# Performance work log

Hardware: AMD Instinct MI355X
Metric: run time of the kernel (lower is better)

## Reference

```python
import jax, jax.numpy as jnp
import numpy as np
import math

N_COARSE, N_FINE = 8192, 32768
DEC_DIM, ENC_DIM, OUT_DIM, K = 256, 128, 128, 16
LN_EPS = 1e-5


def setup_inputs() -> dict:
    key = jax.random.key(0)
    ks = jax.random.split(key, 16)
    s = lambda fan_in: 1.0 / math.sqrt(fan_in)
    return {
        "decoder_features": jax.random.normal(ks[0], (N_COARSE, DEC_DIM), jnp.float32),
        "decoder_pos": jax.random.normal(ks[1], (N_COARSE, 3), jnp.float32),
        "encoder_features": jax.random.normal(ks[2], (N_FINE, ENC_DIM), jnp.float32),
        "encoder_pos": jax.random.normal(ks[3], (N_FINE, 3), jnp.float32),
        "encoder_labels": jax.random.randint(ks[4], (N_FINE,), 0, 13, jnp.int64),
        # params (torch nn.Linear default init scale)
        "Wq": jax.random.uniform(ks[5], (DEC_DIM, ENC_DIM), jnp.float32, -s(ENC_DIM), s(ENC_DIM)),
        "bq": jnp.zeros((DEC_DIM,), jnp.float32),
        "Wk": jax.random.uniform(ks[6], (DEC_DIM, DEC_DIM), jnp.float32, -s(DEC_DIM), s(DEC_DIM)),
        "bk": jnp.zeros((DEC_DIM,), jnp.float32),
        "Wv": jax.random.uniform(ks[7], (DEC_DIM, DEC_DIM), jnp.float32, -s(DEC_DIM), s(DEC_DIM)),
        "bv": jnp.zeros((DEC_DIM,), jnp.float32),
        "W1": jax.random.uniform(ks[8], (OUT_DIM, DEC_DIM + ENC_DIM), jnp.float32, -s(DEC_DIM + ENC_DIM), s(DEC_DIM + ENC_DIM)),
        "b1": jnp.zeros((OUT_DIM,), jnp.float32),
        "W2": jax.random.uniform(ks[9], (OUT_DIM, OUT_DIM), jnp.float32, -s(OUT_DIM), s(OUT_DIM)),
        "b2": jnp.zeros((OUT_DIM,), jnp.float32),
        "ln_g": jnp.ones((OUT_DIM,), jnp.float32),
        "ln_b": jnp.zeros((OUT_DIM,), jnp.float32),
    }


def _knn_indices(encoder_pos, decoder_pos, k):
    # For each fine (encoder) point, k nearest coarse (decoder) points.
    # squared distances [N_fine, N_coarse]
    d2 = (
        jnp.sum(encoder_pos * encoder_pos, axis=1, keepdims=True)
        - 2.0 * encoder_pos @ decoder_pos.T
        + jnp.sum(decoder_pos * decoder_pos, axis=1)[None, :]
    )
    _, idx = jax.lax.top_k(-d2, k)  # [N_fine, K]
    return idx


def reference(decoder_features, decoder_pos, encoder_features, encoder_pos,
              encoder_labels, Wq, bq, Wk, bk, Wv, bv, W1, b1, W2, b2, ln_g, ln_b):
    idx = _knn_indices(encoder_pos, decoder_pos, K)            # [Nf, K]
    nbr = decoder_features[idx]                                 # [Nf, K, Dd]
    query = encoder_features @ Wq.T + bq                        # [Nf, Dd]
    keys = nbr @ Wk.T + bk                                      # [Nf, K, Dd]
    values = nbr @ Wv.T + bv                                    # [Nf, K, Dd]
    scores = jnp.einsum('nd,nkd->nk', query, keys) / math.sqrt(DEC_DIM)
    # segment softmax over edges grouped by fine target == softmax over K
    weights = jax.nn.softmax(scores, axis=-1)                   # [Nf, K]
    agg = jnp.einsum('nk,nkd->nd', weights, values)             # [Nf, Dd]
    combined = jnp.concatenate([agg, encoder_features], axis=-1)
    h = jax.nn.relu(combined @ W1.T + b1)
    up = h @ W2.T + b2                                          # [Nf, out]
    mu = jnp.mean(up, axis=-1, keepdims=True)
    var = jnp.var(up, axis=-1, keepdims=True)
    out = (up - mu) * jax.lax.rsqrt(var + LN_EPS) * ln_g + ln_b
    # dropout is identity in eval mode
    return (out, encoder_pos, encoder_labels)
```

## Files before the change

kernel.cpp:

```cpp
#include <hip/hip_runtime.h>
#include <hip/hip_bf16.h>

typedef __hip_bfloat16 bf16;
typedef unsigned short u16;
typedef float f32x2 __attribute__((ext_vector_type(2)));

#define NC 8192
#define NF 32768
#define KNN 16
#define FMAXV 3.402823466e+38f

__device__ __forceinline__ float bfbits2f(u16 u){
  union { unsigned u; float f; } x; x.u = ((unsigned)u) << 16; return x.f;
}
__device__ __forceinline__ float asfloat(unsigned u){
  union { unsigned u; float f; } x; x.u = u; return x.f;
}
__device__ __forceinline__ f32x2 pk_fma(f32x2 a, f32x2 b, f32x2 c){
  f32x2 d;
  asm("v_pk_fma_f32 %0, %1, %2, %3" : "=v"(d) : "v"(a), "v"(b), "v"(c));
  return d;
}

__global__ __launch_bounds__(256) void k_prep(const float* __restrict__ dpos,
                                              const float* __restrict__ W1,
                                              const float* __restrict__ W2,
                                              float4* __restrict__ posP,
                                              float4* __restrict__ W1eSa,
                                              float4* __restrict__ W1eSb,
                                              float4* __restrict__ W2Sa,
                                              float4* __restrict__ W2Sb){
  int g = blockIdx.x * 256 + threadIdx.x;
  if (g < 4096){
    const float2* dp2 = (const float2*)(dpos + (size_t)g * 6);
    float2 a = dp2[0], b = dp2[1], c = dp2[2];
    float x0 = a.x, y0 = a.y, z0 = b.x;
    float x1 = b.y, y1 = c.x, z1 = c.y;
    float dd0 = __fadd_rn(__fadd_rn(__fmul_rn(x0,x0), __fmul_rn(y0,y0)), __fmul_rn(z0,z0));
    float dd1 = __fadd_rn(__fadd_rn(__fmul_rn(x1,x1), __fmul_rn(y1,y1)), __fmul_rn(z1,z1));
    posP[g * 2]     = make_float4(x0, x1, y0, y1);
    posP[g * 2 + 1] = make_float4(z0, z1, dd0 * 0.5f, dd1 * 0.5f);
  } else if (g >= 8192 && g < 10240){
    int f = g - 8192; int c4 = f >> 6, jg = f & 63;
    W1eSa[f] = ((const float4*)(W1 + (size_t)(2 * jg) * 384 + 256))[c4];
  } else if (g >= 10240 && g < 12288){
    int f = g - 10240; int c4 = f >> 6, jg = f & 63;
    W1eSb[f] = ((const float4*)(W1 + (size_t)(2 * jg + 1) * 384 + 256))[c4];
  } else if (g >= 12288 && g < 14336){
    int f = g - 12288; int c4 = f >> 6, jg = f & 63;
    W2Sa[f] = ((const float4*)(W2 + (size_t)(2 * jg) * 128))[c4];
  } else if (g >= 14336){
    int f = g - 14336; int c4 = f >> 6, jg = f & 63;
    W2Sb[f] = ((const float4*)(W2 + (size_t)(2 * jg + 1) * 128))[c4];
  }
}

__global__ __launch_bounds__(256) void k_wprod(const float* __restrict__ Wk,
                                               const float* __restrict__ Wv,
                                               const float* __restrict__ Wq,
                                               const float* __restrict__ W1,
                                               const float* __restrict__ bk,
                                               const float* __restrict__ bv,
                                               const float* __restrict__ bq,
                                               float* __restrict__ WkqS,
                                               float* __restrict__ WvuS,
                                               float* __restrict__ bkq,
                                               float* __restrict__ bvu,
                                               float* __restrict__ wbq,
                                               float* __restrict__ sbq){
  __shared__ float partial[256];
  __shared__ float red[256];
  int B = blockIdx.x, t = threadIdx.x;
  int csel = B >> 2, tch = B & 3;
  int o = (t & 63) + tch * 64;
  int q = t >> 6;
  int j0 = q * 64;
  if (csel < 128){
    int c = csel;
    float acc = 0.f;
    for (int j = j0; j < j0 + 64; ++j)
      acc = fmaf(Wk[(size_t)j * 256 + o], Wq[(size_t)j * 128 + c], acc);
    partial[t] = acc;
    if (tch == 0) red[t] = bk[t] * Wq[(size_t)t * 128 + c];
    __syncthreads();
    if (t < 64){
      float a = partial[t] + partial[t + 64] + partial[t + 128] + partial[t + 192];
      WkqS[(size_t)((o >> 2) * 128 + c) * 4 + (o & 3)] = a;
    }
    if (tch == 0){
      for (int s = 128; s > 0; s >>= 1){ if (t < s) red[t] += red[t + s]; __syncthreads(); }
      if (t == 0) bkq[c] = red[0];
    }
  } else if (csel < 256){
    int h = csel - 128;
    float acc = 0.f;
    for (int j = j0; j < j0 + 64; ++j)
      acc = fmaf(Wv[(size_t)j * 256 + o], W1[(size_t)h * 384 + j], acc);
    partial[t] = acc;
    if (tch == 0) red[t] = bv[t] * W1[(size_t)h * 384 + t];
    __syncthreads();
    if (t < 64){
      float a = partial[t] + partial[t + 64] + partial[t + 128] + partial[t + 192];
      WvuS[(size_t)((o >> 2) * 128 + h) * 4 + (o & 3)] = a;
    }
    if (tch == 0){
      for (int s = 128; s > 0; s >>= 1){ if (t < s) red[t] += red[t + s]; __syncthreads(); }
      if (t == 0) bvu[h] = red[0];
    }
  } else {
    float acc = 0.f;
    for (int j = j0; j < j0 + 64; ++j)
      acc = fmaf(Wk[(size_t)j * 256 + o], bq[j], acc);
    partial[t] = acc;
    if (tch == 0) red[t] = bk[t] * bq[t];
    __syncthreads();
    if (t < 64){
      float a = partial[t] + partial[t + 64] + partial[t + 128] + partial[t + 192];
      wbq[o] = a;
    }
    if (tch == 0){
      for (int s = 128; s > 0; s >>= 1){ if (t < s) red[t] += red[t + s]; __syncthreads(); }
      if (t == 0) sbq[0] = red[0];
    }
  }
}

__global__ __launch_bounds__(256) void k_dec(const float* __restrict__ df,
                                             const float4* __restrict__ WkqS,
                                             const float4* __restrict__ WvuS,
                                             const float* __restrict__ bkq,
                                             const float* __restrict__ bvu,
                                             const float* __restrict__ wbq,
                                             const float* __restrict__ sbq,
                                             bf16* __restrict__ Zd, bf16* __restrict__ Ud,
                                             float* __restrict__ bqK){
  __shared__ float part[8][32];
  int t = threadIdx.x;
  int g0 = blockIdx.x * 8;
  int half = __builtin_amdgcn_readfirstlane(t >> 7);
  int c = t & 127;
  const float4* W = half ? WvuS : WkqS;
  float acc[8];
  #pragma unroll
  for (int p = 0; p < 8; ++p) acc[p] = 0.f;
  for (int j4 = 0; j4 < 64; ++j4){
    float4 w = W[j4 * 128 + c];
    #pragma unroll
    for (int p = 0; p < 8; ++p){
      float4 a = ((const float4*)(df + (size_t)(g0 + p) * 256))[j4];
      acc[p] += w.x*a.x + w.y*a.y + w.z*a.z + w.w*a.w;
    }
  }
  float bias = half ? bvu[c] : bkq[c];
  bf16* dst = half ? Ud : Zd;
  #pragma unroll
  for (int p = 0; p < 8; ++p)
    dst[(size_t)(g0 + p) * 128 + c] = __float2bfloat16(acc[p] + bias);
  {
    int r = t >> 5, seg = t & 31;
    float s = 0.f;
    const float* dr = df + (size_t)(g0 + r) * 256 + seg * 8;
    const float* wq = wbq + seg * 8;
    #pragma unroll
    for (int e = 0; e < 8; ++e) s = fmaf(dr[e], wq[e], s);
    part[r][seg] = s;
  }
  __syncthreads();
  if (t < 8){
    float s = sbq[0];
    #pragma unroll
    for (int seg = 0; seg < 32; ++seg) s += part[t][seg];
    bqK[g0 + t] = s;
  }
}

__global__ __launch_bounds__(256) void k_knn(const float* __restrict__ epos,
                                             const float4* __restrict__ posP,
                                             int* __restrict__ knnI){
  __shared__ float smin[8 * 64];
  __shared__ float tauLDS[8];
  __shared__ int   cnt[8];
  __shared__ float lval[8][64];
  __shared__ int   lidx[8][64];

  int t = threadIdx.x, lane = t & 63, w = t >> 6;
  int n0 = blockIdx.x * 8;
  f32x2 nex2[8], ney2[8], nez2[8];
  #pragma unroll
  for (int p = 0; p < 8; ++p){
    float nx = -epos[(n0 + p) * 3 + 0];
    float ny = -epos[(n0 + p) * 3 + 1];
    float nz = -epos[(n0 + p) * 3 + 2];
    nex2[p].x = nx; nex2[p].y = nx;
    ney2[p].x = ny; ney2[p].y = ny;
    nez2[p].x = nz; nez2[p].y = nz;
  }
  const float4* base = posP + w * 2048;

  f32x2 vmin2[8];
  #pragma unroll
  for (int p = 0; p < 8; ++p){ vmin2[p].x = FMAXV; vmin2[p].y = FMAXV; }
  #pragma unroll 2
  for (int s = 0; s < 16; ++s){
    int q2 = (s * 64 + lane) * 2;
    float4 XY = base[q2], ZW = base[q2 + 1];
    f32x2 X = {XY.x, XY.y}, Y = {XY.z, XY.w}, Z = {ZW.x, ZW.y}, W = {ZW.z, ZW.w};
    #pragma unroll
    for (int p = 0; p < 8; ++p){
      f32x2 v2 = pk_fma(nex2[p], X, W);
      v2 = pk_fma(ney2[p], Y, v2);
      v2 = pk_fma(nez2[p], Z, v2);
      vmin2[p].x = fminf(vmin2[p].x, v2.x);
      vmin2[p].y = fminf(vmin2[p].y, v2.y);
    }
  }
  float vmin[8];
  #pragma unroll
  for (int p = 0; p < 8; ++p) vmin[p] = fminf(vmin2[p].x, vmin2[p].y);

  #pragma unroll
  for (int k = 2; k <= 64; k <<= 1){
    #pragma unroll
    for (int j = k >> 1; j > 0; j >>= 1){
      bool keepmin = ((lane & j) == 0) == ((lane & k) == 0);
      #pragma unroll
      for (int p = 0; p < 8; ++p){
        float pv = __shfl_xor(vmin[p], j);
        vmin[p] = keepmin ? fminf(vmin[p], pv) : fmaxf(vmin[p], pv);
      }
    }
  }
  if (lane < 16){
    #pragma unroll
    for (int p = 0; p < 8; ++p) smin[p * 64 + w * 16 + lane] = vmin[p];
  }
  if (t < 8) cnt[t] = 0;
  __syncthreads();

  {
    int src = (lane & 16) ? (lane ^ 15) : lane;
    float v0 = smin[(w * 2 + 0) * 64 + src];
    float v1 = smin[(w * 2 + 1) * 64 + src];
    #pragma unroll
    for (int j = 16; j > 0; j >>= 1){
      bool keepmin = ((lane & 32) == 0) == ((lane & j) == 0);
      float p0 = __shfl_xor(v0, j); v0 = keepmin ? fminf(v0, p0) : fmaxf(v0, p0);
      float p1 = __shfl_xor(v1, j); v1 = keepmin ? fminf(v1, p1) : fmaxf(v1, p1);
    }
    #pragma unroll
    for (int j = 32; j > 0; j >>= 1){
      bool keepmin = ((lane & j) == 0);
      float p0 = __shfl_xor(v0, j); v0 = keepmin ? fminf(v0, p0) : fmaxf(v0, p0);
      float p1 = __shfl_xor(v1, j); v1 = keepmin ? fminf(v1, p1) : fmaxf(v1, p1);
    }
    if (lane == 16){ tauLDS[w * 2] = v0; tauLDS[w * 2 + 1] = v1; }
  }
  __syncthreads();
  float tau0[8];
  #pragma unroll
  for (int p = 0; p < 8; ++p) tau0[p] = tauLDS[p];

  #pragma unroll 2
  for (int s = 0; s < 16; ++s){
    int q = s * 64 + lane;
    float4 XY = base[q * 2], ZW = base[q * 2 + 1];
    f32x2 X = {XY.x, XY.y}, Y = {XY.z, XY.w}, Z = {ZW.x, ZW.y}, W = {ZW.z, ZW.w};
    int cand0 = w * 2048 + q * 2;
    #pragma unroll
    for (int p = 0; p < 8; ++p){
      f32x2 v2 = pk_fma(nex2[p], X, W);
      v2 = pk_fma(ney2[p], Y, v2);
      v2 = pk_fma(nez2[p], Z, v2);
      if (v2.x <= tau0[p]){
        int slot = atomicAdd(&cnt[p], 1);
        if (slot < 64){ lval[p][slot] = v2.x; lidx[p][slot] = cand0; }
      }
      if (v2.y <= tau0[p]){
        int slot = atomicAdd(&cnt[p], 1);
        if (slot < 64){ lval[p][slot] = v2.y; lidx[p][slot] = cand0 + 1; }
      }
    }
  }
  __syncthreads();

  {
    int p0 = w * 2, p1 = w * 2 + 1;
    int nA = n0 + p0, nB = n0 + p1;
    int c0 = cnt[p0]; if (c0 > 64) c0 = 64;
    int c1 = cnt[p1]; if (c1 > 64) c1 = 64;
    float va = (lane < c0) ? lval[p0][lane] : FMAXV;
    int   ia = (lane < c0) ? lidx[p0][lane] : 0x7fffffff;
    float vb = (lane < c1) ? lval[p1][lane] : FMAXV;
    int   ib = (lane < c1) ? lidx[p1][lane] : 0x7fffffff;

    #pragma unroll
    for (int k = 2; k <= 16; k <<= 1){
      #pragma unroll
      for (int j = k >> 1; j > 0; j >>= 1){
        bool keepmin = ((lane & k) == 0) == ((lane & j) == 0);
        { float pv = __shfl_xor(va, j); int pid = __shfl_xor(ia, j);
          bool pl = (pv < va) || (pv == va && pid < ia);
          if (keepmin ? pl : !pl){ va = pv; ia = pid; } }
        { float pv = __shfl_xor(vb, j); int pid = __shfl_xor(ib, j);
          bool pl = (pv < vb) || (pv == vb && pid < ib);
          if (keepmin ? pl : !pl){ vb = pv; ib = pid; } }
      }
    }
    { float pv = __shfl_xor(va, 16); int pid = __shfl_xor(ia, 16);
      if ((pv < va) || (pv == va && pid < ia)){ va = pv; ia = pid; } }
    { float pv = __shfl_xor(vb, 16); int pid = __shfl_xor(ib, 16);
      if ((pv < vb) || (pv == vb && pid < ib)){ vb = pv; ib = pid; } }
    #pragma unroll
    for (int j = 8; j > 0; j >>= 1){
      bool keepmin = ((lane & 32) == 0) == ((lane & j) == 0);
      { float pv = __shfl_xor(va, j); int pid = __shfl_xor(ia, j);
        bool pl = (pv < va) || (pv == va && pid < ia);
        if (keepmin ? pl : !pl){ va = pv; ia = pid; } }
      { float pv = __shfl_xor(vb, j); int pid = __shfl_xor(ib, j);
        bool pl = (pv < vb) || (pv == vb && pid < ib);
        if (keepmin ? pl : !pl){ vb = pv; ib = pid; } }
    }
    { float pv = __shfl_xor(va, 32); int pid = __shfl_xor(ia, 32);
      if ((pv < va) || (pv == va && pid < ia)){ va = pv; ia = pid; } }
    { float pv = __shfl_xor(vb, 32); int pid = __shfl_xor(ib, 32);
      if ((pv < vb) || (pv == vb && pid < ib)){ vb = pv; ib = pid; } }

    if (lane < 16){
      knnI[(size_t)nA * 16 + lane] = ia;
      knnI[(size_t)nB * 16 + lane] = ib;
    }
  }
}

__global__ __launch_bounds__(256) void k_amlp(const int* __restrict__ knnI,
                                              const bf16* __restrict__ Zd,
                                              const bf16* __restrict__ Ud,
                                              const float* __restrict__ bqK,
                                              const float* __restrict__ ef,
                                              const float4* __restrict__ W1eSa,
                                              const float4* __restrict__ W1eSb,
                                              const float* __restrict__ b1,
                                              const float4* __restrict__ W2Sa,
                                              const float4* __restrict__ W2Sb,
                                              const float* __restrict__ b2,
                                              const float* __restrict__ lng, const float* __restrict__ lnb,
                                              const float* __restrict__ epos, const int* __restrict__ lab,
                                              float* __restrict__ out){
  __shared__ float haggL[16 * 128];
  __shared__ float hbuf[16 * 128];
  __shared__ float ubuf[16 * 128];
  __shared__ float stats[32];
  int t = threadIdx.x;
  int n0 = blockIdx.x * 16;
  int lane = t & 63, w = t >> 6;
  {
    int gid = blockIdx.x * 256 + t;
    if (gid < NF){
      float* op = out + (size_t)NF * 128;
      op[gid * 3 + 0] = epos[gid * 3 + 0];
      op[gid * 3 + 1] = epos[gid * 3 + 1];
      op[gid * 3 + 2] = epos[gid * 3 + 2];
      out[(size_t)NF * 128 + (size_t)NF * 3 + gid] = (float)lab[gid];
    }
  }

  {
    int kk = lane & 15;
    int pp = w * 4 + (lane >> 4);
    int n = n0 + pp;
    int ik = knnI[(size_t)n * 16 + kk];
    const uint4*  zr = (const uint4*)((const u16*)Zd + (size_t)ik * 128);
    const float4* e4 = (const float4*)(ef + (size_t)n * 128);
    float pr = 0.f;
    #pragma unroll
    for (int i = 0; i < 16; ++i){
      uint4 z = zr[i];
      float4 ea = e4[2 * i], eb = e4[2 * i + 1];
      pr = fmaf(ea.x, asfloat(z.x << 16), pr); pr = fmaf(ea.y, asfloat(z.x & 0xffff0000u), pr);
      pr = fmaf(ea.z, asfloat(z.y << 16), pr); pr = fmaf(ea.w, asfloat(z.y & 0xffff0000u), pr);
      pr = fmaf(eb.x, asfloat(z.z << 16), pr); pr = fmaf(eb.y, asfloat(z.z & 0xffff0000u), pr);
      pr = fmaf(eb.z, asfloat(z.w << 16), pr); pr = fmaf(eb.w, asfloat(z.w & 0xffff0000u), pr);
    }
    float sc = (pr + bqK[ik]) * (1.0f / 16.0f);
    float mx = sc;
    #pragma unroll
    for (int off = 1; off < 16; off <<= 1) mx = fmaxf(mx, __shfl_xor(mx, off));
    float e = __expf(sc - mx);
    float l = e;
    #pragma unroll
    for (int off = 1; off < 16; off <<= 1) l += __shfl_xor(l, off);
    float wgt = e / l;

    float acc8[8];
    #pragma unroll
    for (int j = 0; j < 8; ++j) acc8[j] = 0.f;
    int gbase = lane & 48;
    #pragma unroll
    for (int k2 = 0; k2 < 16; ++k2){
      int src = gbase | k2;
      float wk = __shfl(wgt, src);
      int ikk = __shfl(ik, src);
      uint4 uu = *(const uint4*)((const u16*)Ud + (size_t)ikk * 128 + kk * 8);
      acc8[0] = fmaf(wk, asfloat(uu.x << 16), acc8[0]);
      acc8[1] = fmaf(wk, asfloat(uu.x & 0xffff0000u), acc8[1]);
      acc8[2] = fmaf(wk, asfloat(uu.y << 16), acc8[2]);
      acc8[3] = fmaf(wk, asfloat(uu.y & 0xffff0000u), acc8[3]);
      acc8[4] = fmaf(wk, asfloat(uu.z << 16), acc8[4]);
      acc8[5] = fmaf(wk, asfloat(uu.z & 0xffff0000u), acc8[5]);
      acc8[6] = fmaf(wk, asfloat(uu.w << 16), acc8[6]);
      acc8[7] = fmaf(wk, asfloat(uu.w & 0xffff0000u), acc8[7]);
    }
    float4* hp = (float4*)&haggL[pp * 128 + kk * 8];
    hp[0] = make_float4(acc8[0], acc8[1], acc8[2], acc8[3]);
    hp[1] = make_float4(acc8[4], acc8[5], acc8[6], acc8[7]);
  }

  int jg = t & 63;
  int pg4 = __builtin_amdgcn_readfirstlane((t >> 6) * 4);
  int j0 = jg * 2;
  float acc[2][4];
  #pragma unroll
  for (int a = 0; a < 2; ++a)
    #pragma unroll
    for (int p = 0; p < 4; ++p) acc[a][p] = 0.f;
  for (int c4 = 0; c4 < 32; ++c4){
    float4 wa = W1eSa[c4 * 64 + jg];
    float4 wb = W1eSb[c4 * 64 + jg];
    #pragma unroll
    for (int p = 0; p < 4; ++p){
      float4 x = ((const float4*)(ef + (size_t)(n0 + pg4 + p) * 128))[c4];
      acc[0][p] += wa.x*x.x + wa.y*x.y + wa.z*x.z + wa.w*x.w;
      acc[1][p] += wb.x*x.x + wb.y*x.y + wb.z*x.z + wb.w*x.w;
    }
  }
  __syncthreads();
  float b1a = b1[j0], b1b = b1[j0 + 1];
  #pragma unroll
  for (int p = 0; p < 4; ++p){
    float2 hgv = *(const float2*)&haggL[(pg4 + p) * 128 + j0];
    hbuf[(pg4 + p) * 128 + j0]     = fmaxf(acc[0][p] + b1a + hgv.x, 0.f);
    hbuf[(pg4 + p) * 128 + j0 + 1] = fmaxf(acc[1][p] + b1b + hgv.y, 0.f);
  }
  __syncthreads();
  float acc2[2][4];
  #pragma unroll
  for (int a = 0; a < 2; ++a)
    #pragma unroll
    for (int p = 0; p < 4; ++p) acc2[a][p] = 0.f;
  const float4* hb4 = (const float4*)hbuf;
  for (int c4 = 0; c4 < 32; ++c4){
    float4 wa = W2Sa[c4 * 64 + jg];
    float4 wb = W2Sb[c4 * 64 + jg];
    #pragma unroll
    for (int p = 0; p < 4; ++p){
      float4 x = hb4[(pg4 + p) * 32 + c4];
      acc2[0][p] += wa.x*x.x + wa.y*x.y + wa.z*x.z + wa.w*x.w;
      acc2[1][p] += wb.x*x.x + wb.y*x.y + wb.z*x.z + wb.w*x.w;
    }
  }
  float b2a = b2[j0], b2b = b2[j0 + 1];
  float u[2][4];
  #pragma unroll
  for (int p = 0; p < 4; ++p){
    u[0][p] = acc2[0][p] + b2a;
    u[1][p] = acc2[1][p] + b2b;
    ubuf[(pg4 + p) * 128 + j0]     = u[0][p];
    ubuf[(pg4 + p) * 128 + j0 + 1] = u[1][p];
  }
  __syncthreads();
  {
    int p = t >> 4, qi = t & 15;
    const float* ub = &ubuf[p * 128 + qi * 8];
    float s = 0.f, s2 = 0.f;
    #pragma unroll
    for (int e2i = 0; e2i < 8; ++e2i){ float v = ub[e2i]; s += v; s2 += v * v; }
    #pragma unroll
    for (int off = 1; off < 16; off <<= 1){ s += __shfl_xor(s, off); s2 += __shfl_xor(s2, off); }
    if (qi == 0){
      float mu = s * (1.f / 128.f);
      float var = s2 * (1.f / 128.f) - mu * mu;
      stats[p] = mu;
      stats[16 + p] = rsqrtf(fmaxf(var, 0.f) + 1e-5f);
    }
  }
  __syncthreads();
  float ga = lng[j0], gb = lng[j0 + 1];
  float ba = lnb[j0], bbv = lnb[j0 + 1];
  #pragma unroll
  for (int p = 0; p < 4; ++p){
    float mu = stats[pg4 + p], rs = stats[16 + pg4 + p];
    out[(size_t)(n0 + pg4 + p) * 128 + j0]     = (u[0][p] - mu) * rs * ga + ba;
    out[(size_t)(n0 + pg4 + p) * 128 + j0 + 1] = (u[1][p] - mu) * rs * gb + bbv;
  }
}

extern "C" void kernel_launch(void* const* d_in, const int* in_sizes, int n_in,
                              void* d_out, int out_size, void* d_ws, size_t ws_size,
                              hipStream_t stream){
  const float* df   = (const float*)d_in[0];
  const float* dpos = (const float*)d_in[1];
  const float* ef   = (const float*)d_in[2];
  const float* epos = (const float*)d_in[3];
  const int*   lab  = (const int*)d_in[4];
  const float* Wq = (const float*)d_in[5];
  const float* bq = (const float*)d_in[6];
  const float* Wk = (const float*)d_in[7];
  const float* bk = (const float*)d_in[8];
  const float* Wv = (const float*)d_in[9];
  const float* bv = (const float*)d_in[10];
  const float* W1 = (const float*)d_in[11];
  const float* b1 = (const float*)d_in[12];
  const float* W2 = (const float*)d_in[13];
  const float* b2 = (const float*)d_in[14];
  const float* lng = (const float*)d_in[15];
  const float* lnb = (const float*)d_in[16];
  float* out = (float*)d_out;

  char* wsb = (char*)d_ws;
  float4* posP  = (float4*)(wsb);
  bf16*   Zd    = (bf16*)(wsb + 131072);
  bf16*   Ud    = (bf16*)(wsb + 2228224);
  float*  bqK   = (float*)(wsb + 4325376);
  int*    knnI  = (int*)(wsb + 4358144);
  float4* W1eSa = (float4*)(wsb + 12746752);
  float4* W1eSb = (float4*)(wsb + 12779520);
  float4* W2Sa  = (float4*)(wsb + 12812288);
  float4* W2Sb  = (float4*)(wsb + 12845056);
  float*  WkqS  = (float*)(wsb + 12877824);
  float*  WvuS  = (float*)(wsb + 13008896);
  float*  bkq   = (float*)(wsb + 13139968);
  float*  bvu   = (float*)(wsb + 13140480);
  float*  wbq   = (float*)(wsb + 13140992);
  float*  sbq   = (float*)(wsb + 13142016);

  k_prep  <<<64,   256, 0, stream>>>(dpos, W1, W2, posP, W1eSa, W1eSb, W2Sa, W2Sb);
  k_wprod <<<1028, 256, 0, stream>>>(Wk, Wv, Wq, W1, bk, bv, bq, WkqS, WvuS, bkq, bvu, wbq, sbq);
  k_dec   <<<NC / 8, 256, 0, stream>>>(df, (const float4*)WkqS, (const float4*)WvuS, bkq, bvu, wbq, sbq, Zd, Ud, bqK);
  k_knn   <<<NF / 8, 256, 0, stream>>>(epos, posP, knnI);
  k_amlp  <<<NF / 16, 256, 0, stream>>>(knnI, Zd, Ud, bqK, ef, W1eSa, W1eSb, b1, W2Sa, W2Sb, b2, lng, lnb, epos, lab, out);
  (void)in_sizes; (void)n_in; (void)out_size; (void)ws_size;
}
```

Baseline: 339.7 us.

## Merge prep/wprod and dec/knn kernels into two interleaved-block launches

Fuses the independent position/weight prep kernel with the weight-product kernel, and the decoder projection kernel with the KNN kernel, by assigning block ranges (or every fifth block) to each role. This removes two kernel launches and the idle gaps between them, and lets decoder work overlap with KNN work. Also raises the unroll of the KNN distance loop. The fused kernel carries the shared memory and register demand of both roles, which may lower occupancy.

```diff
diff --git a/kernel.cpp b/kernel.cpp
--- a/kernel.cpp
+++ b/kernel.cpp
@@ -22,55 +22,56 @@
   return d;
 }
 
-__global__ __launch_bounds__(256) void k_prep(const float* __restrict__ dpos,
-                                              const float* __restrict__ W1,
-                                              const float* __restrict__ W2,
-                                              float4* __restrict__ posP,
-                                              float4* __restrict__ W1eSa,
-                                              float4* __restrict__ W1eSb,
-                                              float4* __restrict__ W2Sa,
-                                              float4* __restrict__ W2Sb){
-  int g = blockIdx.x * 256 + threadIdx.x;
-  if (g < 4096){
-    const float2* dp2 = (const float2*)(dpos + (size_t)g * 6);
-    float2 a = dp2[0], b = dp2[1], c = dp2[2];
-    float x0 = a.x, y0 = a.y, z0 = b.x;
-    float x1 = b.y, y1 = c.x, z1 = c.y;
-    float dd0 = __fadd_rn(__fadd_rn(__fmul_rn(x0,x0), __fmul_rn(y0,y0)), __fmul_rn(z0,z0));
-    float dd1 = __fadd_rn(__fadd_rn(__fmul_rn(x1,x1), __fmul_rn(y1,y1)), __fmul_rn(z1,z1));
-    posP[g * 2]     = make_float4(x0, x1, y0, y1);
-    posP[g * 2 + 1] = make_float4(z0, z1, dd0 * 0.5f, dd1 * 0.5f);
-  } else if (g >= 8192 && g < 10240){
-    int f = g - 8192; int c4 = f >> 6, jg = f & 63;
-    W1eSa[f] = ((const float4*)(W1 + (size_t)(2 * jg) * 384 + 256))[c4];
-  } else if (g >= 10240 && g < 12288){
-    int f = g - 10240; int c4 = f >> 6, jg = f & 63;
-    W1eSb[f] = ((const float4*)(W1 + (size_t)(2 * jg + 1) * 384 + 256))[c4];
-  } else if (g >= 12288 && g < 14336){
-    int f = g - 12288; int c4 = f >> 6, jg = f & 63;
-    W2Sa[f] = ((const float4*)(W2 + (size_t)(2 * jg) * 128))[c4];
-  } else if (g >= 14336){
-    int f = g - 14336; int c4 = f >> 6, jg = f & 63;
-    W2Sb[f] = ((const float4*)(W2 + (size_t)(2 * jg + 1) * 128))[c4];
-  }
-}
-
-__global__ __launch_bounds__(256) void k_wprod(const float* __restrict__ Wk,
-                                               const float* __restrict__ Wv,
-                                               const float* __restrict__ Wq,
-                                               const float* __restrict__ W1,
-                                               const float* __restrict__ bk,
-                                               const float* __restrict__ bv,
-                                               const float* __restrict__ bq,
-                                               float* __restrict__ WkqS,
-                                               float* __restrict__ WvuS,
-                                               float* __restrict__ bkq,
-                                               float* __restrict__ bvu,
-                                               float* __restrict__ wbq,
-                                               float* __restrict__ sbq){
+__global__ __launch_bounds__(256) void k_pw(const float* __restrict__ dpos,
+                                            const float* __restrict__ W1,
+                                            const float* __restrict__ W2,
+                                            float4* __restrict__ posP,
+                                            float4* __restrict__ W1eSa,
+                                            float4* __restrict__ W1eSb,
+                                            float4* __restrict__ W2Sa,
+                                            float4* __restrict__ W2Sb,
+                                            const float* __restrict__ Wk,
+                                            const float* __restrict__ Wv,
+                                            const float* __restrict__ Wq,
+                                            const float* __restrict__ bk,
+                                            const float* __restrict__ bv,
+                                            const float* __restrict__ bq,
+                                            float* __restrict__ WkqS,
+                                            float* __restrict__ WvuS,
+                                            float* __restrict__ bkq,
+                                            float* __restrict__ bvu,
+                                            float* __restrict__ wbq,
+                                            float* __restrict__ sbq){
   __shared__ float partial[256];
   __shared__ float red[256];
-  int B = blockIdx.x, t = threadIdx.x;
+  int gb = blockIdx.x, t = threadIdx.x;
+  if (gb >= 1028){
+    int g = (gb - 1028) * 256 + t;
+    if (g < 4096){
+      const float2* dp2 = (const float2*)(dpos + (size_t)g * 6);
+      float2 a = dp2[0], b = dp2[1], c = dp2[2];
+      float x0 = a.x, y0 = a.y, z0 = b.x;
+      float x1 = b.y, y1 = c.x, z1 = c.y;
+      float dd0 = __fadd_rn(__fadd_rn(__fmul_rn(x0,x0), __fmul_rn(y0,y0)), __fmul_rn(z0,z0));
+      float dd1 = __fadd_rn(__fadd_rn(__fmul_rn(x1,x1), __fmul_rn(y1,y1)), __fmul_rn(z1,z1));
+      posP[g * 2]     = make_float4(x0, x1, y0, y1);
+      posP[g * 2 + 1] = make_float4(z0, z1, dd0 * 0.5f, dd1 * 0.5f);
+    } else if (g >= 8192 && g < 10240){
+      int f = g - 8192; int c4 = f >> 6, jg = f & 63;
+      W1eSa[f] = ((const float4*)(W1 + (size_t)(2 * jg) * 384 + 256))[c4];
+    } else if (g >= 10240 && g < 12288){
+      int f = g - 10240; int c4 = f >> 6, jg = f & 63;
+      W1eSb[f] = ((const float4*)(W1 + (size_t)(2 * jg + 1) * 384 + 256))[c4];
+    } else if (g >= 12288 && g < 14336){
+      int f = g - 12288; int c4 = f >> 6, jg = f & 63;
+      W2Sa[f] = ((const float4*)(W2 + (size_t)(2 * jg) * 128))[c4];
+    } else if (g >= 14336 && g < 16384){
+      int f = g - 14336; int c4 = f >> 6, jg = f & 63;
+      W2Sb[f] = ((const float4*)(W2 + (size_t)(2 * jg + 1) * 128))[c4];
+    }
+    return;
+  }
+  int B = gb;
   int csel = B >> 2, tch = B & 3;
   int o = (t & 63) + tch * 64;
   int q = t >> 6;
@@ -125,66 +126,70 @@
   }
 }
 
-__global__ __launch_bounds__(256) void k_dec(const float* __restrict__ df,
-                                             const float4* __restrict__ WkqS,
-                                             const float4* __restrict__ WvuS,
-                                             const float* __restrict__ bkq,
-                                             const float* __restrict__ bvu,
-                                             const float* __restrict__ wbq,
-                                             const float* __restrict__ sbq,
-                                             bf16* __restrict__ Zd, bf16* __restrict__ Ud,
-                                             float* __restrict__ bqK){
-  __shared__ float part[8][32];
-  int t = threadIdx.x;
-  int g0 = blockIdx.x * 8;
-  int half = __builtin_amdgcn_readfirstlane(t >> 7);
-  int c = t & 127;
-  const float4* W = half ? WvuS : WkqS;
-  float acc[8];
-  #pragma unroll
-  for (int p = 0; p < 8; ++p) acc[p] = 0.f;
-  for (int j4 = 0; j4 < 64; ++j4){
-    float4 w = W[j4 * 128 + c];
-    #pragma unroll
-    for (int p = 0; p < 8; ++p){
-      float4 a = ((const float4*)(df + (size_t)(g0 + p) * 256))[j4];
-      acc[p] += w.x*a.x + w.y*a.y + w.z*a.z + w.w*a.w;
-    }
-  }
-  float bias = half ? bvu[c] : bkq[c];
-  bf16* dst = half ? Ud : Zd;
-  #pragma unroll
-  for (int p = 0; p < 8; ++p)
-    dst[(size_t)(g0 + p) * 128 + c] = __float2bfloat16(acc[p] + bias);
-  {
-    int r = t >> 5, seg = t & 31;
-    float s = 0.f;
-    const float* dr = df + (size_t)(g0 + r) * 256 + seg * 8;
-    const float* wq = wbq + seg * 8;
-    #pragma unroll
-    for (int e = 0; e < 8; ++e) s = fmaf(dr[e], wq[e], s);
-    part[r][seg] = s;
-  }
-  __syncthreads();
-  if (t < 8){
-    float s = sbq[0];
-    #pragma unroll
-    for (int seg = 0; seg < 32; ++seg) s += part[t][seg];
-    bqK[g0 + t] = s;
-  }
-}
-
-__global__ __launch_bounds__(256) void k_knn(const float* __restrict__ epos,
-                                             const float4* __restrict__ posP,
-                                             int* __restrict__ knnI){
+__global__ __launch_bounds__(256) void k_dk(const float* __restrict__ df,
+                                            const float4* __restrict__ WkqS,
+                                            const float4* __restrict__ WvuS,
+                                            const float* __restrict__ bkq,
+                                            const float* __restrict__ bvu,
+                                            const float* __restrict__ wbq,
+                                            const float* __restrict__ sbq,
+                                            bf16* __restrict__ Zd, bf16* __restrict__ Ud,
+                                            float* __restrict__ bqK,
+                                            const float* __restrict__ epos,
+                                            const float4* __restrict__ posP,
+                                            int* __restrict__ knnI){
+  __shared__ float dpart[8][32];
   __shared__ float smin[8 * 64];
   __shared__ float tauLDS[8];
   __shared__ int   cnt[8];
   __shared__ float lval[8][64];
   __shared__ int   lidx[8][64];
 
-  int t = threadIdx.x, lane = t & 63, w = t >> 6;
-  int n0 = blockIdx.x * 8;
+  int g = blockIdx.x, t = threadIdx.x;
+  int m = g % 5, q5 = g / 5;
+  if (m == 4){
+    int g0 = q5 * 8;
+    int half = __builtin_amdgcn_readfirstlane(t >> 7);
+    int c = t & 127;
+    const float4* W = half ? WvuS : WkqS;
+    float acc[8];
+    #pragma unroll
+    for (int p = 0; p < 8; ++p) acc[p] = 0.f;
+    for (int j4 = 0; j4 < 64; ++j4){
+      float4 w = W[j4 * 128 + c];
+      #pragma unroll
+      for (int p = 0; p < 8; ++p){
+        float4 a = ((const float4*)(df + (size_t)(g0 + p) * 256))[j4];
+        acc[p] += w.x*a.x + w.y*a.y + w.z*a.z + w.w*a.w;
+      }
+    }
+    float bias = half ? bvu[c] : bkq[c];
+    bf16* dst = half ? Ud : Zd;
+    #pragma unroll
+    for (int p = 0; p < 8; ++p)
+      dst[(size_t)(g0 + p) * 128 + c] = __float2bfloat16(acc[p] + bias);
+    {
+      int r = t >> 5, seg = t & 31;
+      float s = 0.f;
+      const float* dr = df + (size_t)(g0 + r) * 256 + seg * 8;
+      const float* wq = wbq + seg * 8;
+      #pragma unroll
+      for (int e = 0; e < 8; ++e) s = fmaf(dr[e], wq[e], s);
+      dpart[r][seg] = s;
+    }
+    __syncthreads();
+    if (t < 8){
+      float s = sbq[0];
+      #pragma unroll
+      for (int seg = 0; seg < 32; ++seg) s += dpart[t][seg];
+      bqK[g0 + t] = s;
+    }
+    return;
+  }
+
+  int kb = q5 * 4 + m;
+  int lane = t & 63, w = t >> 6;
+  int n0 = kb * 8;
   f32x2 nex2[8], ney2[8], nez2[8];
   #pragma unroll
   for (int p = 0; p < 8; ++p){
@@ -200,7 +205,7 @@
   f32x2 vmin2[8];
   #pragma unroll
   for (int p = 0; p < 8; ++p){ vmin2[p].x = FMAXV; vmin2[p].y = FMAXV; }
-  #pragma unroll 2
+  #pragma unroll 4
   for (int s = 0; s < 16; ++s){
     int q2 = (s * 64 + lane) * 2;
     float4 XY = base[q2], ZW = base[q2 + 1];
@@ -533,10 +538,10 @@
   float*  wbq   = (float*)(wsb + 13140992);
   float*  sbq   = (float*)(wsb + 13142016);
 
-  k_prep  <<<64,   256, 0, stream>>>(dpos, W1, W2, posP, W1eSa, W1eSb, W2Sa, W2Sb);
-  k_wprod <<<1028, 256, 0, stream>>>(Wk, Wv, Wq, W1, bk, bv, bq, WkqS, WvuS, bkq, bvu, wbq, sbq);
-  k_dec   <<<NC / 8, 256, 0, stream>>>(df, (const float4*)WkqS, (const float4*)WvuS, bkq, bvu, wbq, sbq, Zd, Ud, bqK);
-  k_knn   <<<NF / 8, 256, 0, stream>>>(epos, posP, knnI);
-  k_amlp  <<<NF / 16, 256, 0, stream>>>(knnI, Zd, Ud, bqK, ef, W1eSa, W1eSb, b1, W2Sa, W2Sb, b2, lng, lnb, epos, lab, out);
+  k_pw   <<<1092, 256, 0, stream>>>(dpos, W1, W2, posP, W1eSa, W1eSb, W2Sa, W2Sb,
+                                    Wk, Wv, Wq, bk, bv, bq, WkqS, WvuS, bkq, bvu, wbq, sbq);
+  k_dk   <<<5120, 256, 0, stream>>>(df, (const float4*)WkqS, (const float4*)WvuS, bkq, bvu, wbq, sbq,
+                                    Zd, Ud, bqK, epos, posP, knnI);
+  k_amlp <<<NF / 16, 256, 0, stream>>>(knnI, Zd, Ud, bqK, ef, W1eSa, W1eSb, b1, W2Sa, W2Sb, b2, lng, lnb, epos, lab, out);
   (void)in_sizes; (void)n_in; (void)out_size; (void)ws_size;
 }
```

Result: no change. 333.5 us (-1.8%).
